# Performance work log

Hardware: AMD Instinct MI355X
Metric: run time of the kernel (lower is better)

The kernel has to match this reference:

```python
import jax, jax.numpy as jnp
import numpy as np

V, P = 50000, 50
WE, PE = 300, 100
LH = 800            # bidirectional total hidden
H = LH // 2         # per-direction hidden = 400
MH = 1024           # mlp_hidden_dim
B, T = 32, 128


def setup_inputs() -> dict:
    key = jax.random.key(0)
    ks = jax.random.split(key, 16)
    s = 0.05
    inp = {
        "word_tensor": jax.random.randint(ks[0], (B, T), 0, V, dtype=jnp.int32),
        "word_lengths": jnp.full((B,), T, dtype=jnp.int32),
        "pos_tensor": jax.random.randint(ks[1], (B, T), 0, P, dtype=jnp.int32),
        "word_emb": jax.random.normal(ks[2], (V, WE), jnp.float32) * s,
        "pos_emb": jax.random.normal(ks[3], (P, PE), jnp.float32) * s,
        # LSTM layer 0: input dim WE+PE=400; stacked over 2 directions
        "Wih0": jax.random.normal(ks[4], (2, 4 * H, WE + PE), jnp.float32) * s,
        "Whh0": jax.random.normal(ks[5], (2, 4 * H, H), jnp.float32) * s,
        "b0": jnp.zeros((2, 4 * H), jnp.float32),
        # LSTM layer 1: input dim = 2*H = 800
        "Wih1": jax.random.normal(ks[6], (2, 4 * H, LH), jnp.float32) * s,
        "Whh1": jax.random.normal(ks[7], (2, 4 * H, H), jnp.float32) * s,
        "b1": jnp.zeros((2, 4 * H), jnp.float32),
        "Wh": jax.random.normal(ks[8], (MH // 2, LH), jnp.float32) * s,
        "bh": jnp.zeros((MH // 2,), jnp.float32),
        "Wm": jax.random.normal(ks[9], (MH // 2, LH), jnp.float32) * s,
        "bm": jnp.zeros((MH // 2,), jnp.float32),
        "Wo": jax.random.normal(ks[10], (1, MH), jnp.float32) * s,
        "bo": jnp.zeros((1,), jnp.float32),
    }
    return inp


def _lstm_dir(x_tbd, W_ih, W_hh, bias, reverse):
    # x_tbd: [T,B,D]; PyTorch gate order i,f,g,o
    Bsz = x_tbd.shape[1]
    Hd = W_hh.shape[1]
    def cell(carry, xt):
        h, c = carry
        g = xt @ W_ih.T + h @ W_hh.T + bias
        i, f, gg, o = jnp.split(g, 4, axis=-1)
        c = jax.nn.sigmoid(f) * c + jax.nn.sigmoid(i) * jnp.tanh(gg)
        h = jax.nn.sigmoid(o) * jnp.tanh(c)
        return (h, c), h
    init = (jnp.zeros((Bsz, Hd), x_tbd.dtype), jnp.zeros((Bsz, Hd), x_tbd.dtype))
    _, hs = jax.lax.scan(cell, init, x_tbd, reverse=reverse)
    return hs  # [T,B,H], in original time order


def _bilstm_layer(x_btd, Wih, Whh, b):
    x_tbd = jnp.swapaxes(x_btd, 0, 1)
    fwd = _lstm_dir(x_tbd, Wih[0], Whh[0], b[0], reverse=False)
    bwd = _lstm_dir(x_tbd, Wih[1], Whh[1], b[1], reverse=True)
    out = jnp.concatenate([fwd, bwd], axis=-1)  # [T,B,2H]
    return jnp.swapaxes(out, 0, 1)              # [B,T,2H]


def reference(word_tensor, word_lengths, pos_tensor, word_emb, pos_emb,
              Wih0, Whh0, b0, Wih1, Whh1, b1,
              Wh, bh, Wm, bm, Wo, bo):
    embeds = jnp.concatenate([word_emb[word_tensor], pos_emb[pos_tensor]], axis=2)  # [B,T,400]
    h1 = _bilstm_layer(embeds, Wih0, Whh0, b0)   # [B,T,800]
    lstm_out = _bilstm_layer(h1, Wih1, Whh1, b1)  # [B,T,800]
    head_f = lstm_out @ Wh.T + bh   # [B,T,512]
    modif_f = lstm_out @ Wm.T + bm  # [B,T,512]
    # score[b,h,m] = Wo @ tanh(cat(head_f[b,h], modif_f[b,m])) + bo
    # tanh(cat(a,b)) = cat(tanh(a), tanh(b)) -> exact decomposition
    half = Wo.shape[1] // 2
    s_h = jnp.tanh(head_f) @ Wo[0, :half]   # [B,T]
    s_m = jnp.tanh(modif_f) @ Wo[0, half:]  # [B,T]
    score = s_h[:, :, None] + s_m[:, None, :] + bo[0]  # [B,T,T]
    return score
```

## Files before the change

### kernel.cpp

```cpp
#include <hip/hip_runtime.h>

#define DEV __device__ __forceinline__

typedef _Float16 f16;
typedef _Float16 f16x8 __attribute__((ext_vector_type(8)));
typedef float f32x4 __attribute__((ext_vector_type(4)));
typedef unsigned long long ull;

static constexpr int K0P  = 416;
static constexpr int NBLK = 13;
static constexpr int GN   = 3328;
static constexpr int WKP  = 424;
static constexpr int HXP  = 13 * 2560;
static constexpr int SMEM_LSTM = 2 * HXP + 64;
static constexpr int HB1_ELEM  = 2 * 128 * 13 * 1024;
static constexpr int HB_BYTES  = 2 * HB1_ELEM * 2;
static constexpr unsigned READY0 = 0x80008000u;

DEV float sigf(float x) { return 1.f / (1.f + __expf(-x)); }
DEV float tanhf_(float x) {
  x = fminf(10.f, fmaxf(-10.f, x));
  float e = __expf(2.f * x);
  return (e - 1.f) / (e + 1.f);
}
DEV ull  AL8(const ull* p) { return __hip_atomic_load(p, __ATOMIC_RELAXED, __HIP_MEMORY_SCOPE_AGENT); }
DEV void AS4(unsigned* p, unsigned v) { __hip_atomic_store(p, v, __ATOMIC_RELAXED, __HIP_MEMORY_SCOPE_AGENT); }


__global__ void embed_k(const int* __restrict__ wt, const int* __restrict__ pt,
                        const float* __restrict__ we, const float* __restrict__ pe,
                        f16* __restrict__ x0)
{
  const int r = blockIdx.x;
  const int tid = threadIdx.x;
  const int w = wt[r], p = pt[r];
  const float* wrow = we + (size_t)w * 300;
  const float* prow = pe + (size_t)p * 100;
  f16* xr = x0 + (size_t)r * K0P;
  for (int k = tid; k < K0P; k += 128) {
    float v = (k < 300) ? wrow[k] : (k < 400 ? prow[k - 300] : 0.f);
    xr[k] = (f16)v;
  }
}

__global__ void convpad_k(const float* __restrict__ src, f16* __restrict__ dst,
                          int rows, int K, int KP)
{
  const size_t total = (size_t)rows * KP;
  for (size_t i = (size_t)blockIdx.x * blockDim.x + threadIdx.x; i < total;
       i += (size_t)gridDim.x * blockDim.x) {
    int r = (int)(i / KP), k = (int)(i % KP);
    dst[i] = (f16)(k < K ? src[(size_t)r * K + k] : 0.f);
  }
}

__global__ void wih_reorder_k(const float* __restrict__ src, const float* __restrict__ bias,
                              f16* __restrict__ dst, float* __restrict__ biasr,
                              int K, int KP)
{
  const size_t total = (size_t)GN * KP;
  for (size_t i = (size_t)blockIdx.x * blockDim.x + threadIdx.x; i < total;
       i += (size_t)gridDim.x * blockDim.x) {
    int k = (int)(i % KP);
    int R = (int)(i / KP);
    int d = R / 1664, rr = R % 1664, blk = rr >> 7, loc = rr & 127;
    int w = loc >> 5, t = (loc >> 4) & 1, fq = (loc >> 2) & 3, g = loc & 3;
    int u = blk * 32 + w * 8 + 2 * fq + t;
    float v = (u < 400 && k < K) ? src[((size_t)d * 1600 + g * 400 + u) * K + k] : 0.f;
    dst[i] = (f16)v;
    if (k == 0) biasr[R] = (u < 400) ? bias[d * 1600 + g * 400 + u] : 0.f;
  }
}

__global__ void whh_reorder_k(const float* __restrict__ src, f16* __restrict__ dst)
{
  const int total = 2 * NBLK * 128 * WKP;
  for (int i = blockIdx.x * blockDim.x + threadIdx.x; i < total;
       i += gridDim.x * blockDim.x) {
    int k = i % WKP, loc = (i / WKP) & 127, blk = (i / (WKP * 128)) % NBLK,
        d = i / (WKP * 128 * NBLK);
    int w = loc >> 5, t = (loc >> 4) & 1, fq = (loc >> 2) & 3, g = loc & 3;
    int u = blk * 32 + w * 8 + 2 * fq + t;
    float v = (u < 400 && k < 400) ? src[((size_t)d * 1600 + g * 400 + u) * 400 + k] : 0.f;
    dst[i] = (f16)v;
  }
}

__global__ void biascat_k(const float* __restrict__ bh, const float* __restrict__ bm,
                          float* __restrict__ bhm)
{
  int i = threadIdx.x;
  bhm[i] = i < 512 ? bh[i] : bm[i - 512];
}

__global__ void init_hb_k(unsigned* __restrict__ p, int n)
{
  for (int i = blockIdx.x * blockDim.x + threadIdx.x; i < n; i += gridDim.x * blockDim.x) {
    int off = i % (13 * 512);
    int blk = off >> 9, win = off & 511;
    bool pad = (blk == 12) && ((win >> 7) & 1);
    AS4(p + i, pad ? READY0 : 0u);
  }
}

__global__ __launch_bounds__(256) void unpack_k(const f16* __restrict__ hBl,
                                                f16* __restrict__ h_out)
{
  const int d = blockIdx.x >> 7, s = blockIdx.x & 127;
  const int t = d ? 127 - s : s;
  const unsigned* slab = (const unsigned*)(hBl + ((size_t)d * 128 + s) * 13 * 1024);
  for (int j = threadIdx.x; j < 13 * 512; j += 256) {
    const int blk = j >> 9, q = j & 511, half = q >> 8, q2 = q & 255;
    const int fq = q2 & 3, fr = (q2 >> 2) & 15, w = q2 >> 6;
    const int u0 = blk * 32 + w * 8 + 2 * fq;
    if (u0 < 400) {
      const int b = fr + 16 * half;
      *(unsigned*)(h_out + (size_t)(b * 128 + t) * 800 + d * 400 + u0) = slab[j];
    }
  }
}

__global__ __launch_bounds__(256) void gemm_f16_nt(
    const f16* __restrict__ A, const f16* __restrict__ Bw,
    const float* __restrict__ bias, float* __restrict__ C,
    int M, int N, int KP)
{
  __shared__ __align__(16) f16 As[128][40];
  __shared__ __align__(16) f16 Bs[128][40];
  const int tid = threadIdx.x;
  const int bn = blockIdx.x, bm = blockIdx.y;
  const int lane = tid & 63, wid = tid >> 6;
  const int wr = wid >> 1, wc = wid & 1;
  const int srow = tid >> 1, shalf = tid & 1;
  const f16* Ap = A + (size_t)(bm * 128 + srow) * KP + shalf * 16;
  const f16* Bp = Bw + (size_t)(bn * 128 + srow) * KP + shalf * 16;
  const int fr = lane & 15, fq = lane >> 4;
  f32x4 acc[4][4] = {};
  for (int kt = 0; kt < KP; kt += 32) {
    __syncthreads();
    *(uint4*)&As[srow][shalf * 16]     = *(const uint4*)(Ap + kt);
    *(uint4*)&As[srow][shalf * 16 + 8] = *(const uint4*)(Ap + kt + 8);
    *(uint4*)&Bs[srow][shalf * 16]     = *(const uint4*)(Bp + kt);
    *(uint4*)&Bs[srow][shalf * 16 + 8] = *(const uint4*)(Bp + kt + 8);
    __syncthreads();
    f16x8 af[4], bf[4];
    #pragma unroll
    for (int m = 0; m < 4; ++m) af[m] = *(const f16x8*)&As[wr * 64 + m * 16 + fr][fq * 8];
    #pragma unroll
    for (int n = 0; n < 4; ++n) bf[n] = *(const f16x8*)&Bs[wc * 64 + n * 16 + fr][fq * 8];
    #pragma unroll
    for (int m = 0; m < 4; ++m)
      #pragma unroll
      for (int n = 0; n < 4; ++n)
        acc[m][n] = __builtin_amdgcn_mfma_f32_16x16x32_f16(af[m], bf[n], acc[m][n], 0, 0, 0);
  }
  #pragma unroll
  for (int n = 0; n < 4; ++n) {
    const int gn = bn * 128 + wc * 64 + n * 16 + fr;
    const float bv = bias ? bias[gn] : 0.f;
    #pragma unroll
    for (int m = 0; m < 4; ++m) {
      const size_t gm = (size_t)bm * 128 + wr * 64 + m * 16 + fq * 4;
      #pragma unroll
      for (int r = 0; r < 4; ++r)
        C[(gm + r) * (size_t)N + gn] = acc[m][n][r] + bv;
    }
  }
}

__global__ __launch_bounds__(256, 1) void lstm_mfma_k(
    const float* __restrict__ gates,
    const f16* __restrict__ whh_r,
    f16* __restrict__ hB)
{
  extern __shared__ __align__(16) char smem[];
  char* hx   = smem;
  int*  flds = (int*)(smem + 2 * HXP);

  const int d = blockIdx.x / NBLK, blk = blockIdx.x % NBLK;
  const int tid = threadIdx.x;
  const int lane = tid & 63, w = tid >> 6;
  const int fr = lane & 15, fq = lane >> 4;

  if (tid < 13) flds[tid] = -1;

  const f16* wr0 = whh_r + ((size_t)(d * NBLK + blk) * 128 + w * 32 + fr) * WKP + fq * 8;
  const f16* wr1 = wr0 + (size_t)16 * WKP;
  f16x8 a0r[13], a1r[13];
  #pragma unroll
  for (int kk = 0; kk < 13; ++kk) {
    a0r[kk] = *(const f16x8*)(wr0 + kk * 32);
    a1r[kk] = *(const f16x8*)(wr1 + kk * 32);
  }

  const int u0 = blk * 32 + w * 8 + 2 * fq;
  const bool ok = u0 < 400;
  const float* gbase0 = gates + (size_t)(fr * 128) * GN + d * 1664 + blk * 128 + w * 32;
  const float* gbase1 = gbase0 + (size_t)16 * 128 * GN;
  f16* hb_d = hB + (size_t)d * 128 * 13 * 1024;
  const int nkk = (w == 0) ? 4 : 3;
  const int kk0 = (w == 0) ? 0 : 4 + 3 * (w - 1);
  const unsigned ownfull = (1u << nkk) - 1;

  float c00 = 0.f, c01 = 0.f, c10 = 0.f, c11 = 0.f;
  float4 pc00, pc10, pc01, pc11;
  {
    const int t0 = d ? 127 : 0;
    const float* g0 = gbase0 + (size_t)t0 * GN;
    const float* g1 = gbase1 + (size_t)t0 * GN;
    pc00 = *(const float4*)(g0 + fq * 4);
    pc10 = *(const float4*)(g0 + 16 + fq * 4);
    pc01 = *(const float4*)(g1 + fq * 4);
    pc11 = *(const float4*)(g1 + 16 + fq * 4);
  }
  __syncthreads();

  for (int s = 0; s < 128; ++s) {
    f32x4 acc00 = {}, acc01 = {}, acc10 = {}, acc11 = {};
    if (s > 0) {
      const ull* slab = (const ull*)(hb_d + (size_t)(s - 1) * 13 * 1024) + lane * 2;
      char* hxw = hx + (s & 1) * HXP;
      ull q[4][4];
      unsigned pend = (nkk == 4) ? 0xFFFFu : 0x0FFFu;
      unsigned stagedm = 0;
      unsigned flagged = 0;
      unsigned done = 0;
      while (done != 0x1FFFu) {
        bool progress = false;
        if (flagged != ownfull) {
          #pragma unroll
          for (int i = 0; i < 4; ++i)
            if (i < nkk && !((flagged >> i) & 1)) {
              const ull* pp = slab + (kk0 + i) * 256;
              if ((pend >> (i * 4 + 0)) & 1) q[i][0] = AL8(pp);
              if ((pend >> (i * 4 + 1)) & 1) q[i][1] = AL8(pp + 1);
              if ((pend >> (i * 4 + 2)) & 1) q[i][2] = AL8(pp + 128);
              if ((pend >> (i * 4 + 3)) & 1) q[i][3] = AL8(pp + 129);
            }
          __builtin_amdgcn_sched_barrier(0);
          #pragma unroll
          for (int i = 0; i < 4; ++i)
            if (i < nkk && !((flagged >> i) & 1)) {
              #pragma unroll
              for (int j = 0; j < 4; ++j)
                if ((pend >> (i * 4 + j)) & 1) {
                  ull v = q[i][j];
                  if ((unsigned)v != 0u && (unsigned)(v >> 32) != 0u)
                    pend &= ~(1u << (i * 4 + j));
                }
              if (!((stagedm >> i) & 1) && ((pend >> (i * 4)) & 15u) == 0u) {
                char* hp = hxw + (kk0 + i) * 2560 + lane * 40;
                *(ull*)(hp +  0) = q[i][0];
                *(ull*)(hp +  8) = q[i][1];
                *(ull*)(hp + 16) = q[i][2];
                *(ull*)(hp + 24) = q[i][3];
                stagedm |= 1u << i;
              }
              bool dn = (stagedm >> i) & 1;
              if (__all(dn)) {
                asm volatile("s_waitcnt lgkmcnt(0)" ::: "memory");
                if (lane == 0)
                  __hip_atomic_store(&flds[kk0 + i], s, __ATOMIC_RELAXED,
                                     __HIP_MEMORY_SCOPE_WORKGROUP);
                flagged |= 1u << i;
                progress = true;
              }
            }
        }
        {
          int fv = (lane < 13)
                     ? __hip_atomic_load(&flds[lane], __ATOMIC_RELAXED,
                                         __HIP_MEMORY_SCOPE_WORKGROUP)
                     : 0x7fffffff;
          unsigned rdy = (unsigned)__ballot(fv >= s) & 0x1FFFu;
          unsigned todo = rdy & ~done;
          if (todo) {
            progress = true;
            #pragma unroll
            for (int kk = 0; kk < 13; ++kk)
              if ((todo >> kk) & 1) {
                const char* hp = hxw + kk * 2560 + lane * 40;
                union { ull u[2]; f16x8 v; } B0, B1;
                B0.u[0] = *(const ull*)(hp);      B0.u[1] = *(const ull*)(hp + 8);
                B1.u[0] = *(const ull*)(hp + 16); B1.u[1] = *(const ull*)(hp + 24);
                acc00 = __builtin_amdgcn_mfma_f32_16x16x32_f16(a0r[kk], B0.v, acc00, 0, 0, 0);
                acc01 = __builtin_amdgcn_mfma_f32_16x16x32_f16(a0r[kk], B1.v, acc01, 0, 0, 0);
                acc10 = __builtin_amdgcn_mfma_f32_16x16x32_f16(a1r[kk], B0.v, acc10, 0, 0, 0);
                acc11 = __builtin_amdgcn_mfma_f32_16x16x32_f16(a1r[kk], B1.v, acc11, 0, 0, 0);
              }
            done |= todo;
          }
        }
        if (!progress && done != 0x1FFFu) __builtin_amdgcn_s_sleep(1);
      }
    }

    float4 pn00 = pc00, pn10 = pc10, pn01 = pc01, pn11 = pc11;
    if (s < 127) {
      const int tn = d ? 126 - s : s + 1;
      const float* g0 = gbase0 + (size_t)tn * GN;
      const float* g1 = gbase1 + (size_t)tn * GN;
      pn00 = *(const float4*)(g0 + fq * 4);
      pn10 = *(const float4*)(g0 + 16 + fq * 4);
      pn01 = *(const float4*)(g1 + fq * 4);
      pn11 = *(const float4*)(g1 + 16 + fq * 4);
    }

    __syncthreads();

    auto act = [&](const f32x4& a, const float4& p, float& c) -> f16 {
      float vi = a[0] + p.x, vf = a[1] + p.y, vg = a[2] + p.z, vo = a[3] + p.w;
      c = sigf(vf) * c + sigf(vi) * tanhf_(vg);
      return (f16)(sigf(vo) * tanhf_(c));
    };
    f16 h00 = act(acc00, pc00, c00);
    f16 h10 = act(acc10, pc10, c10);
    f16 h01 = act(acc01, pc01, c01);
    f16 h11 = act(acc11, pc11, c11);

    if (ok) {
      unsigned pk0 = (unsigned)__builtin_bit_cast(unsigned short, h00) |
                     ((unsigned)__builtin_bit_cast(unsigned short, h10) << 16);
      unsigned pk1 = (unsigned)__builtin_bit_cast(unsigned short, h01) |
                     ((unsigned)__builtin_bit_cast(unsigned short, h11) << 16);
      if (pk0 == 0u) pk0 = READY0;
      if (pk1 == 0u) pk1 = READY0;
      unsigned* hbw = (unsigned*)(hb_d + (size_t)s * 13 * 1024 + blk * 1024
                                  + (w * 16 + fr) * 8) + fq;
      AS4(hbw, pk0);
      AS4(hbw + 256, pk1);
    }
    pc00 = pn00; pc10 = pn10; pc01 = pn01; pc11 = pn11;
  }
}

__global__ __launch_bounds__(256) void tail_k(const float* __restrict__ feat,
                                              const float* __restrict__ wo,
                                              float* __restrict__ s_h,
                                              float* __restrict__ s_m)
{
  const int r = blockIdx.x;
  const int tid = threadIdx.x;
  const float* fr = feat + (size_t)r * 1024;
  float sum = 0.f;
  const int n0 = tid * 4;
  #pragma unroll
  for (int j = 0; j < 4; ++j) sum += tanhf_(fr[n0 + j]) * wo[n0 + j];
  #pragma unroll
  for (int off = 32; off > 0; off >>= 1) sum += __shfl_down(sum, off, 64);
  __shared__ float red[4];
  if ((tid & 63) == 0) red[tid >> 6] = sum;
  __syncthreads();
  if (tid == 0)       s_h[r] = red[0] + red[1];
  else if (tid == 64) s_m[r] = red[2] + red[3];
}

__global__ void score_k(const float* __restrict__ s_h, const float* __restrict__ s_m,
                        const float* __restrict__ bo, float* __restrict__ out)
{
  const int bh = blockIdx.x;
  const int m = threadIdx.x;
  out[(size_t)bh * 128 + m] = s_h[bh] + s_m[(bh & ~127) + m] + bo[0];
}

extern "C" void kernel_launch(void* const* d_in, const int* in_sizes, int n_in,
                              void* d_out, int out_size, void* d_ws, size_t ws_size,
                              hipStream_t stream)
{
  const int*   wt   = (const int*)d_in[0];
  const int*   pt   = (const int*)d_in[2];
  const float* we   = (const float*)d_in[3];
  const float* pe   = (const float*)d_in[4];
  const float* Wih0 = (const float*)d_in[5];
  const float* Whh0 = (const float*)d_in[6];
  const float* b0   = (const float*)d_in[7];
  const float* Wih1 = (const float*)d_in[8];
  const float* Whh1 = (const float*)d_in[9];
  const float* b1   = (const float*)d_in[10];
  const float* Wh   = (const float*)d_in[11];
  const float* bh   = (const float*)d_in[12];
  const float* Wm   = (const float*)d_in[13];
  const float* bm   = (const float*)d_in[14];
  const float* Wo   = (const float*)d_in[15];
  const float* bo   = (const float*)d_in[16];
  float* out = (float*)d_out;

  char* p = (char*)d_ws;
  auto alloc = [&](size_t bytes) { char* q = p; p += (bytes + 255) & ~(size_t)255; return q; };
  f16*   x0    = (f16*)alloc((size_t)4096 * K0P * 2);
  f16*   wihr0 = (f16*)alloc((size_t)GN * K0P * 2);
  f16*   wihr1 = (f16*)alloc((size_t)GN * 800 * 2);
  f16*   whhr0 = (f16*)alloc((size_t)2 * NBLK * 128 * WKP * 2);
  f16*   whhr1 = (f16*)alloc((size_t)2 * NBLK * 128 * WKP * 2);
  f16*   whm   = (f16*)alloc((size_t)1024 * 800 * 2);
  float* biasr0= (float*)alloc(GN * 4);
  float* biasr1= (float*)alloc(GN * 4);
  float* bhm   = (float*)alloc(1024 * 4);
  float* sh    = (float*)alloc(4096 * 4);
  float* sm    = (float*)alloc(4096 * 4);
  f16*   h1    = (f16*)alloc((size_t)4096 * 800 * 2);
  f16*   h2    = (f16*)alloc((size_t)4096 * 800 * 2);
  f16*   hB    = (f16*)alloc(HB_BYTES);
  float* gates = (float*)alloc((size_t)4096 * GN * 4);
  float* feat  = (float*)gates;

  static bool attr_set = false;
  if (!attr_set) {
    hipFuncSetAttribute((const void*)lstm_mfma_k,
                        hipFuncAttributeMaxDynamicSharedMemorySize, SMEM_LSTM);
    attr_set = true;
  }

  init_hb_k<<<512, 256, 0, stream>>>((unsigned*)hB, HB_BYTES / 4);
  embed_k<<<4096, 128, 0, stream>>>(wt, pt, we, pe, x0);
  wih_reorder_k<<<1024, 256, 0, stream>>>(Wih0, b0, wihr0, biasr0, 400, K0P);
  wih_reorder_k<<<1024, 256, 0, stream>>>(Wih1, b1, wihr1, biasr1, 800, 800);
  whh_reorder_k<<<1024, 256, 0, stream>>>(Whh0, whhr0);
  whh_reorder_k<<<1024, 256, 0, stream>>>(Whh1, whhr1);
  convpad_k<<<1024, 256, 0, stream>>>(Wh, whm, 512, 800, 800);
  convpad_k<<<1024, 256, 0, stream>>>(Wm, whm + (size_t)512 * 800, 512, 800, 800);
  biascat_k<<<1, 1024, 0, stream>>>(bh, bm, bhm);

  gemm_f16_nt<<<dim3(26, 32), 256, 0, stream>>>(x0, wihr0, biasr0, gates, 4096, GN, K0P);
  lstm_mfma_k<<<26, 256, SMEM_LSTM, stream>>>(gates, whhr0, hB);
  unpack_k<<<256, 256, 0, stream>>>(hB, h1);
  gemm_f16_nt<<<dim3(26, 32), 256, 0, stream>>>(h1, wihr1, biasr1, gates, 4096, GN, 800);
  lstm_mfma_k<<<26, 256, SMEM_LSTM, stream>>>(gates, whhr1, hB + HB1_ELEM);
  unpack_k<<<256, 256, 0, stream>>>(hB + HB1_ELEM, h2);
  gemm_f16_nt<<<dim3(8, 32), 256, 0, stream>>>(h2, whm, bhm, feat, 4096, 1024, 800);
  tail_k<<<4096, 256, 0, stream>>>(feat, Wo, sh, sm);
  score_k<<<4096, 128, 0, stream>>>(sh, sm, bo, out);
}
```

Before: 1.624 ms.

## Run both LSTM directions in one block per slice, interleaving steps

The recurrent LSTM kernel now launches 13 blocks, each handling the same hidden slice for both forward and backward directions, instead of 26 blocks with one direction each. Within a time step the block processes one direction while the other direction's data from peer blocks is still arriving, so cross-block latency is hidden. The fine-grained overlap of partial MFMA accumulation with flag arrival is replaced by waiting for all slices, then doing the full matmul. Register pressure doubles, since weights for both directions are held in registers. Per-step work per block also doubles.

```diff
diff --git a/kernel.cpp b/kernel.cpp
--- a/kernel.cpp
+++ b/kernel.cpp
@@ -12,7 +12,7 @@
 static constexpr int GN   = 3328;
 static constexpr int WKP  = 424;
 static constexpr int HXP  = 13 * 2560;
-static constexpr int SMEM_LSTM = 2 * HXP + 64;
+static constexpr int SMEM_LSTM = 2 * HXP + 128;
 static constexpr int HB1_ELEM  = 2 * 128 * 13 * 1024;
 static constexpr int HB_BYTES  = 2 * HB1_ELEM * 2;
 static constexpr unsigned READY0 = 0x80008000u;
@@ -168,66 +168,71 @@
   }
 }
 
-__global__ __launch_bounds__(256, 1) void lstm_mfma_k(
+__global__ __launch_bounds__(256, 1) void lstm_dual_k(
     const float* __restrict__ gates,
     const f16* __restrict__ whh_r,
     f16* __restrict__ hB)
 {
   extern __shared__ __align__(16) char smem[];
-  char* hx   = smem;
+  char* hx0  = smem;
+  char* hx1  = smem + HXP;
   int*  flds = (int*)(smem + 2 * HXP);
 
-  const int d = blockIdx.x / NBLK, blk = blockIdx.x % NBLK;
+  const int blk = blockIdx.x;
   const int tid = threadIdx.x;
   const int lane = tid & 63, w = tid >> 6;
   const int fr = lane & 15, fq = lane >> 4;
 
-  if (tid < 13) flds[tid] = -1;
-
-  const f16* wr0 = whh_r + ((size_t)(d * NBLK + blk) * 128 + w * 32 + fr) * WKP + fq * 8;
-  const f16* wr1 = wr0 + (size_t)16 * WKP;
-  f16x8 a0r[13], a1r[13];
-  #pragma unroll
-  for (int kk = 0; kk < 13; ++kk) {
-    a0r[kk] = *(const f16x8*)(wr0 + kk * 32);
-    a1r[kk] = *(const f16x8*)(wr1 + kk * 32);
+  if (tid < 32) flds[tid] = -1;
+
+  f16x8 af[2][2][13];
+  #pragma unroll
+  for (int dd = 0; dd < 2; ++dd) {
+    const f16* wr0 = whh_r + ((size_t)(dd * NBLK + blk) * 128 + w * 32 + fr) * WKP + fq * 8;
+    #pragma unroll
+    for (int kk = 0; kk < 13; ++kk) {
+      af[dd][0][kk] = *(const f16x8*)(wr0 + kk * 32);
+      af[dd][1][kk] = *(const f16x8*)(wr0 + (size_t)16 * WKP + kk * 32);
+    }
   }
 
   const int u0 = blk * 32 + w * 8 + 2 * fq;
   const bool ok = u0 < 400;
-  const float* gbase0 = gates + (size_t)(fr * 128) * GN + d * 1664 + blk * 128 + w * 32;
-  const float* gbase1 = gbase0 + (size_t)16 * 128 * GN;
-  f16* hb_d = hB + (size_t)d * 128 * 13 * 1024;
   const int nkk = (w == 0) ? 4 : 3;
   const int kk0 = (w == 0) ? 0 : 4 + 3 * (w - 1);
   const unsigned ownfull = (1u << nkk) - 1;
 
-  float c00 = 0.f, c01 = 0.f, c10 = 0.f, c11 = 0.f;
-  float4 pc00, pc10, pc01, pc11;
-  {
-    const int t0 = d ? 127 : 0;
-    const float* g0 = gbase0 + (size_t)t0 * GN;
-    const float* g1 = gbase1 + (size_t)t0 * GN;
-    pc00 = *(const float4*)(g0 + fq * 4);
-    pc10 = *(const float4*)(g0 + 16 + fq * 4);
-    pc01 = *(const float4*)(g1 + fq * 4);
-    pc11 = *(const float4*)(g1 + 16 + fq * 4);
+  const float* gb[2][2];
+  #pragma unroll
+  for (int dd = 0; dd < 2; ++dd) {
+    gb[dd][0] = gates + (size_t)(fr * 128) * GN + dd * 1664 + blk * 128 + w * 32;
+    gb[dd][1] = gb[dd][0] + (size_t)16 * 128 * GN;
+  }
+  float  c_[2][4] = {};
+  float4 gp[2][4];
+  #pragma unroll
+  for (int dd = 0; dd < 2; ++dd) {
+    const int t0 = dd ? 127 : 0;
+    gp[dd][0] = *(const float4*)(gb[dd][0] + (size_t)t0 * GN + fq * 4);
+    gp[dd][1] = *(const float4*)(gb[dd][0] + (size_t)t0 * GN + 16 + fq * 4);
+    gp[dd][2] = *(const float4*)(gb[dd][1] + (size_t)t0 * GN + fq * 4);
+    gp[dd][3] = *(const float4*)(gb[dd][1] + (size_t)t0 * GN + 16 + fq * 4);
   }
   __syncthreads();
 
   for (int s = 0; s < 128; ++s) {
-    f32x4 acc00 = {}, acc01 = {}, acc10 = {}, acc11 = {};
-    if (s > 0) {
-      const ull* slab = (const ull*)(hb_d + (size_t)(s - 1) * 13 * 1024) + lane * 2;
-      char* hxw = hx + (s & 1) * HXP;
-      ull q[4][4];
-      unsigned pend = (nkk == 4) ? 0xFFFFu : 0x0FFFu;
-      unsigned stagedm = 0;
-      unsigned flagged = 0;
-      unsigned done = 0;
-      while (done != 0x1FFFu) {
-        bool progress = false;
-        if (flagged != ownfull) {
+    #pragma unroll
+    for (int dd = 0; dd < 2; ++dd) {
+      char* hxw = dd ? hx1 : hx0;
+      int*  fld = flds + dd * 16;
+      f32x4 acc00 = {}, acc01 = {}, acc10 = {}, acc11 = {};
+      if (s > 0) {
+        const ull* slab = (const ull*)(hB + ((size_t)dd * 128 + (s - 1)) * 13 * 1024) + lane * 2;
+        ull q[4][4];
+        unsigned pend = (nkk == 4) ? 0xFFFFu : 0x0FFFu;
+        unsigned stagedm = 0, flagged = 0;
+        int rnd = 0;
+        while (flagged != ownfull) {
           #pragma unroll
           for (int i = 0; i < 4; ++i)
             if (i < nkk && !((flagged >> i) & 1)) {
@@ -260,77 +265,68 @@
               if (__all(dn)) {
                 asm volatile("s_waitcnt lgkmcnt(0)" ::: "memory");
                 if (lane == 0)
-                  __hip_atomic_store(&flds[kk0 + i], s, __ATOMIC_RELAXED,
+                  __hip_atomic_store(&fld[kk0 + i], s, __ATOMIC_RELAXED,
                                      __HIP_MEMORY_SCOPE_WORKGROUP);
                 flagged |= 1u << i;
-                progress = true;
               }
             }
+          if (flagged != ownfull && ++rnd >= 2) __builtin_amdgcn_s_sleep(1);
         }
-        {
+        for (;;) {
           int fv = (lane < 13)
-                     ? __hip_atomic_load(&flds[lane], __ATOMIC_RELAXED,
+                     ? __hip_atomic_load(&fld[lane], __ATOMIC_RELAXED,
                                          __HIP_MEMORY_SCOPE_WORKGROUP)
                      : 0x7fffffff;
-          unsigned rdy = (unsigned)__ballot(fv >= s) & 0x1FFFu;
-          unsigned todo = rdy & ~done;
-          if (todo) {
-            progress = true;
-            #pragma unroll
-            for (int kk = 0; kk < 13; ++kk)
-              if ((todo >> kk) & 1) {
-                const char* hp = hxw + kk * 2560 + lane * 40;
-                union { ull u[2]; f16x8 v; } B0, B1;
-                B0.u[0] = *(const ull*)(hp);      B0.u[1] = *(const ull*)(hp + 8);
-                B1.u[0] = *(const ull*)(hp + 16); B1.u[1] = *(const ull*)(hp + 24);
-                acc00 = __builtin_amdgcn_mfma_f32_16x16x32_f16(a0r[kk], B0.v, acc00, 0, 0, 0);
-                acc01 = __builtin_amdgcn_mfma_f32_16x16x32_f16(a0r[kk], B1.v, acc01, 0, 0, 0);
-                acc10 = __builtin_amdgcn_mfma_f32_16x16x32_f16(a1r[kk], B0.v, acc10, 0, 0, 0);
-                acc11 = __builtin_amdgcn_mfma_f32_16x16x32_f16(a1r[kk], B1.v, acc11, 0, 0, 0);
-              }
-            done |= todo;
-          }
+          if (!__any(fv < s)) break;
+          __builtin_amdgcn_s_sleep(1);
         }
-        if (!progress && done != 0x1FFFu) __builtin_amdgcn_s_sleep(1);
+        asm volatile("" ::: "memory");
+        #pragma unroll
+        for (int kk = 0; kk < 13; ++kk) {
+          const char* hp = hxw + kk * 2560 + lane * 40;
+          union { ull u[2]; f16x8 v; } B0, B1;
+          B0.u[0] = *(const ull*)(hp);      B0.u[1] = *(const ull*)(hp + 8);
+          B1.u[0] = *(const ull*)(hp + 16); B1.u[1] = *(const ull*)(hp + 24);
+          acc00 = __builtin_amdgcn_mfma_f32_16x16x32_f16(af[dd][0][kk], B0.v, acc00, 0, 0, 0);
+          acc01 = __builtin_amdgcn_mfma_f32_16x16x32_f16(af[dd][0][kk], B1.v, acc01, 0, 0, 0);
+          acc10 = __builtin_amdgcn_mfma_f32_16x16x32_f16(af[dd][1][kk], B0.v, acc10, 0, 0, 0);
+          acc11 = __builtin_amdgcn_mfma_f32_16x16x32_f16(af[dd][1][kk], B1.v, acc11, 0, 0, 0);
+        }
       }
+
+      float4 g0 = gp[dd][0], g1 = gp[dd][1], g2 = gp[dd][2], g3 = gp[dd][3];
+      if (s < 127) {
+        const int tn = dd ? 126 - s : s + 1;
+        gp[dd][0] = *(const float4*)(gb[dd][0] + (size_t)tn * GN + fq * 4);
+        gp[dd][1] = *(const float4*)(gb[dd][0] + (size_t)tn * GN + 16 + fq * 4);
+        gp[dd][2] = *(const float4*)(gb[dd][1] + (size_t)tn * GN + fq * 4);
+        gp[dd][3] = *(const float4*)(gb[dd][1] + (size_t)tn * GN + 16 + fq * 4);
+      }
+
+      auto act = [&](const f32x4& a, const float4& p, float& c) -> f16 {
+        float vi = a[0] + p.x, vf = a[1] + p.y, vg = a[2] + p.z, vo = a[3] + p.w;
+        c = sigf(vf) * c + sigf(vi) * tanhf_(vg);
+        return (f16)(sigf(vo) * tanhf_(c));
+      };
+      f16 h00 = act(acc00, g0, c_[dd][0]);
+      f16 h10 = act(acc10, g1, c_[dd][1]);
+      f16 h01 = act(acc01, g2, c_[dd][2]);
+      f16 h11 = act(acc11, g3, c_[dd][3]);
+
+      if (ok) {
+        unsigned pk0 = (unsigned)__builtin_bit_cast(unsigned short, h00) |
+                       ((unsigned)__builtin_bit_cast(unsigned short, h10) << 16);
+        unsigned pk1 = (unsigned)__builtin_bit_cast(unsigned short, h01) |
+                       ((unsigned)__builtin_bit_cast(unsigned short, h11) << 16);
+        if (pk0 == 0u) pk0 = READY0;
+        if (pk1 == 0u) pk1 = READY0;
+        unsigned* hbw = (unsigned*)(hB + ((size_t)dd * 128 + s) * 13 * 1024 + blk * 1024
+                                    + (w * 16 + fr) * 8) + fq;
+        AS4(hbw, pk0);
+        AS4(hbw + 256, pk1);
+      }
+      __syncthreads();
     }
-
-    float4 pn00 = pc00, pn10 = pc10, pn01 = pc01, pn11 = pc11;
-    if (s < 127) {
-      const int tn = d ? 126 - s : s + 1;
-      const float* g0 = gbase0 + (size_t)tn * GN;
-      const float* g1 = gbase1 + (size_t)tn * GN;
-      pn00 = *(const float4*)(g0 + fq * 4);
-      pn10 = *(const float4*)(g0 + 16 + fq * 4);
-      pn01 = *(const float4*)(g1 + fq * 4);
-      pn11 = *(const float4*)(g1 + 16 + fq * 4);
-    }
-
-    __syncthreads();
-
-    auto act = [&](const f32x4& a, const float4& p, float& c) -> f16 {
-      float vi = a[0] + p.x, vf = a[1] + p.y, vg = a[2] + p.z, vo = a[3] + p.w;
-      c = sigf(vf) * c + sigf(vi) * tanhf_(vg);
-      return (f16)(sigf(vo) * tanhf_(c));
-    };
-    f16 h00 = act(acc00, pc00, c00);
-    f16 h10 = act(acc10, pc10, c10);
-    f16 h01 = act(acc01, pc01, c01);
-    f16 h11 = act(acc11, pc11, c11);
-
-    if (ok) {
-      unsigned pk0 = (unsigned)__builtin_bit_cast(unsigned short, h00) |
-                     ((unsigned)__builtin_bit_cast(unsigned short, h10) << 16);
-      unsigned pk1 = (unsigned)__builtin_bit_cast(unsigned short, h01) |
-                     ((unsigned)__builtin_bit_cast(unsigned short, h11) << 16);
-      if (pk0 == 0u) pk0 = READY0;
-      if (pk1 == 0u) pk1 = READY0;
-      unsigned* hbw = (unsigned*)(hb_d + (size_t)s * 13 * 1024 + blk * 1024
-                                  + (w * 16 + fr) * 8) + fq;
-      AS4(hbw, pk0);
-      AS4(hbw + 256, pk1);
-    }
-    pc00 = pn00; pc10 = pn10; pc01 = pn01; pc11 = pn11;
   }
 }
 
@@ -406,7 +402,7 @@
 
   static bool attr_set = false;
   if (!attr_set) {
-    hipFuncSetAttribute((const void*)lstm_mfma_k,
+    hipFuncSetAttribute((const void*)lstm_dual_k,
                         hipFuncAttributeMaxDynamicSharedMemorySize, SMEM_LSTM);
     attr_set = true;
   }
@@ -422,10 +418,10 @@
   biascat_k<<<1, 1024, 0, stream>>>(bh, bm, bhm);
 
   gemm_f16_nt<<<dim3(26, 32), 256, 0, stream>>>(x0, wihr0, biasr0, gates, 4096, GN, K0P);
-  lstm_mfma_k<<<26, 256, SMEM_LSTM, stream>>>(gates, whhr0, hB);
+  lstm_dual_k<<<NBLK, 256, SMEM_LSTM, stream>>>(gates, whhr0, hB);
   unpack_k<<<256, 256, 0, stream>>>(hB, h1);
   gemm_f16_nt<<<dim3(26, 32), 256, 0, stream>>>(h1, wihr1, biasr1, gates, 4096, GN, 800);
-  lstm_mfma_k<<<26, 256, SMEM_LSTM, stream>>>(gates, whhr1, hB + HB1_ELEM);
+  lstm_dual_k<<<NBLK, 256, SMEM_LSTM, stream>>>(gates, whhr1, hB + HB1_ELEM);
   unpack_k<<<256, 256, 0, stream>>>(hB + HB1_ELEM, h2);
   gemm_f16_nt<<<dim3(8, 32), 256, 0, stream>>>(h2, whm, bhm, feat, 4096, 1024, 800);
   tail_k<<<4096, 256, 0, stream>>>(feat, Wo, sh, sm);
```

Measured after the change: 2.123 ms. 1.31x slower.
